# Optimization experiments

Hardware: AMD Instinct MI355X
Metric: run time of the kernel (lower is better)

## Reference

```python
import jax, jax.numpy as jnp
import numpy as np

LN_EPS = 1e-5


def setup_inputs() -> dict:
    key = jax.random.key(0)
    k0, k1, k2, k3 = jax.random.split(key, 4)
    b, X, Y, w1, w2, d = 16, 16, 16, 8, 8, 128
    heads = 4
    x = jax.random.normal(k0, (b, X, Y, w1, w2, d), dtype=jnp.float32)
    gamma = jnp.ones((d,), dtype=jnp.float32)
    beta = jnp.zeros((d,), dtype=jnp.float32)
    w_qkv = jax.random.normal(k1, (d, 3 * d), dtype=jnp.float32) * 0.02
    w_out = jax.random.normal(k2, (d, d), dtype=jnp.float32) * 0.02
    bias_table = jax.random.normal(k3, ((2 * w1 - 1) * (2 * w2 - 1), heads), dtype=jnp.float32) * 0.02
    return {"x": x, "gamma": gamma, "beta": beta, "w_qkv": w_qkv,
            "w_out": w_out, "bias_table": bias_table,
            "window_height": 8, "window_width": 8}


def _rel_pos_indices(wh, ww):
    gh = jnp.arange(wh)
    gw = jnp.arange(ww)
    grid = jnp.stack(jnp.meshgrid(gh, gw, indexing='ij'), axis=-1).reshape(-1, 2)  # [n, 2]
    rel = grid[:, None, :] - grid[None, :, :]  # [n, n, 2]
    rel = rel + jnp.array([wh - 1, ww - 1])
    return rel[..., 0] * (2 * ww - 1) + rel[..., 1]  # [n, n]


def reference(x, gamma, beta, w_qkv, w_out, bias_table, window_height, window_width):
    b, X, Y, w1, w2, d = x.shape
    heads = bias_table.shape[-1]
    dh = d // heads
    scale = dh ** -0.5

    # LayerNorm over channel dim
    mu = x.mean(axis=-1, keepdims=True)
    var = jnp.mean((x - mu) ** 2, axis=-1, keepdims=True)
    xn = (x - mu) * jax.lax.rsqrt(var + LN_EPS) * gamma + beta

    n = w1 * w2
    xn = xn.reshape(b * X * Y, n, d)  # [B, n, d], B = b*X*Y windows

    qkv = xn @ w_qkv  # [B, n, 3d]
    q, k, v = jnp.split(qkv, 3, axis=-1)
    def split_heads(t):
        return t.reshape(t.shape[0], n, heads, dh).transpose(0, 2, 1, 3)  # [B, h, n, dh]
    q, k, v = map(split_heads, (q, k, v))

    sim = jnp.einsum('bhid,bhjd->bhij', q * scale, k)  # [B, h, n, n]

    idx = _rel_pos_indices(window_height, window_width)  # [n, n]
    bias = bias_table[idx].transpose(2, 0, 1)  # [h, n, n]

    attn = jax.nn.softmax(sim + bias, axis=-1)
    out = jnp.einsum('bhij,bhjd->bhid', attn, v)  # [B, h, n, dh]
    out = out.transpose(0, 2, 1, 3).reshape(b * X * Y, w1, w2, d)
    out = out @ w_out
    return out.reshape(b, X, Y, w1, w2, d)
```

## Files before the change

kernel.cpp:

```cpp
#include <hip/hip_runtime.h>

typedef __attribute__((ext_vector_type(4))) short short4v;
typedef __attribute__((ext_vector_type(8))) short short8;
typedef __attribute__((ext_vector_type(4))) float f32x4;

#define NWIN 4096

__device__ __forceinline__ short f2bf(float f) {
    unsigned int u = __builtin_bit_cast(unsigned int, f);
    u += 0x7fffu + ((u >> 16) & 1u);
    return (short)(u >> 16);
}

__device__ __forceinline__ unsigned pack2(float a, float b) {
    return (unsigned)(unsigned short)f2bf(a) | ((unsigned)(unsigned short)f2bf(b) << 16);
}

__device__ __forceinline__ short4v pk4(float a, float b, float c, float d) {
    uint2 u;
    u.x = pack2(a, b);
    u.y = pack2(c, d);
    return __builtin_bit_cast(short4v, u);
}

#define LOG2E 1.4426950408889634f
#define QSCALE 0.17677669529663687f

__global__ void prep_kernel(const float* __restrict__ w_qkv,
                            const float* __restrict__ w_out,
                            const float* __restrict__ bias_table,
                            short* __restrict__ wqkvT,
                            short* __restrict__ woutT,
                            float* __restrict__ biasP)
{
    int id = blockIdx.x * 256 + threadIdx.x;
    if (id < 49152) {
        int j = id >> 7, k = id & 127;
        float v = w_qkv[k * 384 + j];
        if (j < 128) v *= (QSCALE * LOG2E);
        wqkvT[id] = f2bf(v);
    } else if (id < 65536) {
        int t = id - 49152;
        int j = t >> 7, k = t & 127;
        woutT[t] = f2bf(w_out[k * 128 + j]);
    } else if (id < 81920) {
        int t = id - 65536;
        int m  = t & 15;
        int ln = (t >> 4) & 63;
        int ib = (t >> 10) & 3;
        int h  = t >> 12;
        int lo = ln & 15, g = ln >> 4;
        int i = ib * 16 + lo;
        int j = (m >> 2) * 16 + g * 4 + (m & 3);
        int ri = i >> 3, ci = i & 7, rj = j >> 3, cj = j & 7;
        int idx = (ri - rj + 7) * 15 + (ci - cj + 7);
        biasP[t] = bias_table[idx * 4 + h] * LOG2E;
    }
}

__global__ __launch_bounds__(256, 2)
void attn_kernel(const float* __restrict__ x,
                 const float* __restrict__ gamma,
                 const float* __restrict__ beta,
                 const short* __restrict__ wqkvT,
                 const short* __restrict__ woutT,
                 const float* __restrict__ biasP,
                 float* __restrict__ out)
{
    __shared__ __align__(16) char smem[32768];

    const int tid = threadIdx.x;
    const int h  = tid >> 6;
    const int ln = tid & 63;
    const int lo = ln & 15, g = ln >> 4;

    const float* xwin = x + (size_t)blockIdx.x * 8192;

    float4 va[4][2];
    #pragma unroll
    for (int p = 0; p < 4; ++p) {
        int t = h * 16 + p * 4 + g;
        const float4* xr = (const float4*)(xwin + t * 128 + lo * 8);
        va[p][0] = xr[0];
        va[p][1] = xr[1];
    }
    float4 ga0 = ((const float4*)gamma)[lo * 2], ga1 = ((const float4*)gamma)[lo * 2 + 1];
    float4 be0 = ((const float4*)beta)[lo * 2],  be1 = ((const float4*)beta)[lo * 2 + 1];

    #pragma unroll
    for (int p = 0; p < 4; ++p) {
        int t = h * 16 + p * 4 + g;
        float4 v0 = va[p][0], v1 = va[p][1];
        float s  = v0.x + v0.y + v0.z + v0.w + v1.x + v1.y + v1.z + v1.w;
        float sq = v0.x*v0.x + v0.y*v0.y + v0.z*v0.z + v0.w*v0.w
                 + v1.x*v1.x + v1.y*v1.y + v1.z*v1.z + v1.w*v1.w;
        #pragma unroll
        for (int m = 1; m < 16; m <<= 1) {
            s  += __shfl_xor(s, m, 64);
            sq += __shfl_xor(sq, m, 64);
        }
        float mu  = s * (1.f / 128.f);
        float var = sq * (1.f / 128.f) - mu * mu;
        float rs  = rsqrtf(var + 1e-5f);
        float y0 = (v0.x - mu) * rs * ga0.x + be0.x;
        float y1 = (v0.y - mu) * rs * ga0.y + be0.y;
        float y2 = (v0.z - mu) * rs * ga0.z + be0.z;
        float y3 = (v0.w - mu) * rs * ga0.w + be0.w;
        float y4 = (v1.x - mu) * rs * ga1.x + be1.x;
        float y5 = (v1.y - mu) * rs * ga1.y + be1.y;
        float y6 = (v1.z - mu) * rs * ga1.z + be1.z;
        float y7 = (v1.w - mu) * rs * ga1.w + be1.w;
        uint4 pk;
        pk.x = pack2(y0, y1); pk.y = pack2(y2, y3);
        pk.z = pack2(y4, y5); pk.w = pack2(y6, y7);
        *(uint4*)(smem + ((t * 256 + lo * 16) ^ ((t & 7) << 4))) = pk;
    }
    __syncthreads();

    const f32x4 z4 = {0.f, 0.f, 0.f, 0.f};

    f32x4 qt[2][4], kt[2][4];
    #pragma unroll
    for (int a = 0; a < 2; ++a)
        #pragma unroll
        for (int b = 0; b < 4; ++b) { qt[a][b] = z4; kt[a][b] = z4; }

    #pragma unroll
    for (int kk = 0; kk < 4; ++kk) {
        short8 xa[4];
        #pragma unroll
        for (int tb = 0; tb < 4; ++tb) {
            int t = tb * 16 + lo;
            xa[tb] = *(const short8*)(smem + ((t * 256 + kk * 64 + g * 16) ^ ((t & 7) << 4)));
        }
        #pragma unroll
        for (int cb = 0; cb < 2; ++cb) {
            short8 wqf = *(const short8*)(wqkvT + (      h * 32 + cb * 16 + lo) * 128 + kk * 32 + g * 8);
            short8 wkf = *(const short8*)(wqkvT + (128 + h * 32 + cb * 16 + lo) * 128 + kk * 32 + g * 8);
            #pragma unroll
            for (int tb = 0; tb < 4; ++tb) {
                qt[cb][tb] = __builtin_amdgcn_mfma_f32_16x16x32_bf16(wqf, xa[tb], qt[cb][tb], 0, 0, 0);
                kt[cb][tb] = __builtin_amdgcn_mfma_f32_16x16x32_bf16(wkf, xa[tb], kt[cb][tb], 0, 0, 0);
            }
        }
    }

    short4v kA[2][4], qB[2][4];
    #pragma unroll
    for (int ck = 0; ck < 2; ++ck)
        #pragma unroll
        for (int tb = 0; tb < 4; ++tb) {
            kA[ck][tb] = pk4(kt[ck][tb][0], kt[ck][tb][1], kt[ck][tb][2], kt[ck][tb][3]);
            qB[ck][tb] = pk4(qt[ck][tb][0], qt[ck][tb][1], qt[ck][tb][2], qt[ck][tb][3]);
        }

    f32x4 vv[4][2];
    #pragma unroll
    for (int a = 0; a < 4; ++a)
        #pragma unroll
        for (int b = 0; b < 2; ++b) vv[a][b] = z4;

    #pragma unroll
    for (int kk = 0; kk < 4; ++kk) {
        short8 xa[4];
        #pragma unroll
        for (int tb = 0; tb < 4; ++tb) {
            int t = tb * 16 + lo;
            xa[tb] = *(const short8*)(smem + ((t * 256 + kk * 64 + g * 16) ^ ((t & 7) << 4)));
        }
        #pragma unroll
        for (int cb = 0; cb < 2; ++cb) {
            short8 wvf = *(const short8*)(wqkvT + (256 + h * 32 + cb * 16 + lo) * 128 + kk * 32 + g * 8);
            #pragma unroll
            for (int tb = 0; tb < 4; ++tb)
                vv[tb][cb] = __builtin_amdgcn_mfma_f32_16x16x32_bf16(xa[tb], wvf, vv[tb][cb], 0, 0, 0);
        }
    }

    char* vtb = smem + 16384 + h * 4096;
    #pragma unroll
    for (int cb = 0; cb < 2; ++cb)
        #pragma unroll
        for (int tb = 0; tb < 4; ++tb) {
            int c = cb * 16 + lo;
            uint2 w;
            w.x = pack2(vv[tb][cb][0], vv[tb][cb][1]);
            w.y = pack2(vv[tb][cb][2], vv[tb][cb][3]);
            *(uint2*)(vtb + ((c * 128 + tb * 32 + g * 8) ^ ((c & 7) << 4))) = w;
        }

    f32x4 ot[2][4];
    #pragma unroll
    for (int a = 0; a < 2; ++a)
        #pragma unroll
        for (int b = 0; b < 4; ++b) ot[a][b] = z4;

    float inv[4];
    #pragma unroll
    for (int ib = 0; ib < 4; ++ib) {
        f32x4 bias_cur[4];
        {
            const f32x4* bp = (const f32x4*)(biasP + ((h * 4 + ib) * 64 + ln) * 16);
            #pragma unroll
            for (int jb = 0; jb < 4; ++jb) bias_cur[jb] = bp[jb];
        }

        f32x4 st[4];
        #pragma unroll
        for (int jb = 0; jb < 4; ++jb) st[jb] = z4;
        #pragma unroll
        for (int jb = 0; jb < 4; ++jb) {
            st[jb] = __builtin_amdgcn_mfma_f32_16x16x16bf16_1k(kA[0][jb], qB[0][ib], st[jb], 0, 0, 0);
            st[jb] = __builtin_amdgcn_mfma_f32_16x16x16bf16_1k(kA[1][jb], qB[1][ib], st[jb], 0, 0, 0);
        }

        float v[16];
        #pragma unroll
        for (int jb = 0; jb < 4; ++jb)
            #pragma unroll
            for (int r = 0; r < 4; ++r)
                v[jb * 4 + r] = st[jb][r] + bias_cur[jb][r];
        float mx = v[0];
        #pragma unroll
        for (int q = 1; q < 16; ++q) mx = fmaxf(mx, v[q]);
        mx = fmaxf(mx, __shfl_xor(mx, 16, 64));
        mx = fmaxf(mx, __shfl_xor(mx, 32, 64));
        float s = 0.f;
        #pragma unroll
        for (int q = 0; q < 16; ++q) { v[q] = __builtin_exp2f(v[q] - mx); s += v[q]; }
        s += __shfl_xor(s, 16, 64);
        s += __shfl_xor(s, 32, 64);
        inv[ib] = 1.f / s;

        short4v pB[4];
        #pragma unroll
        for (int jk = 0; jk < 4; ++jk)
            pB[jk] = pk4(v[jk * 4 + 0], v[jk * 4 + 1], v[jk * 4 + 2], v[jk * 4 + 3]);

        #pragma unroll
        for (int jk = 0; jk < 4; ++jk)
            #pragma unroll
            for (int cb = 0; cb < 2; ++cb) {
                int c = cb * 16 + lo;
                short4v vA = __builtin_bit_cast(short4v,
                    *(const uint2*)(vtb + ((c * 128 + jk * 32 + g * 8) ^ ((c & 7) << 4))));
                ot[cb][ib] = __builtin_amdgcn_mfma_f32_16x16x16bf16_1k(vA, pB[jk], ot[cb][ib], 0, 0, 0);
            }
    }
    __syncthreads();

    #pragma unroll
    for (int cb = 0; cb < 2; ++cb)
        #pragma unroll
        for (int ib = 0; ib < 4; ++ib) {
            int i = ib * 16 + lo;
            float sc = inv[ib];
            uint2 w;
            w.x = pack2(ot[cb][ib][0] * sc, ot[cb][ib][1] * sc);
            w.y = pack2(ot[cb][ib][2] * sc, ot[cb][ib][3] * sc);
            *(uint2*)(smem + ((i * 256 + (h * 32 + cb * 16 + g * 4) * 2) ^ ((i & 7) << 4))) = w;
        }
    __syncthreads();

    f32x4 ft[2][4];
    #pragma unroll
    for (int a = 0; a < 2; ++a)
        #pragma unroll
        for (int b = 0; b < 4; ++b) ft[a][b] = z4;

    #pragma unroll
    for (int kk = 0; kk < 4; ++kk) {
        short8 ao[4];
        #pragma unroll
        for (int tb = 0; tb < 4; ++tb) {
            int t = tb * 16 + lo;
            ao[tb] = *(const short8*)(smem + ((t * 256 + kk * 64 + g * 16) ^ ((t & 7) << 4)));
        }
        #pragma unroll
        for (int cj = 0; cj < 2; ++cj) {
            short8 wof = *(const short8*)(woutT + (h * 32 + cj * 16 + lo) * 128 + kk * 32 + g * 8);
            #pragma unroll
            for (int tb = 0; tb < 4; ++tb)
                ft[cj][tb] = __builtin_amdgcn_mfma_f32_16x16x32_bf16(wof, ao[tb], ft[cj][tb], 0, 0, 0);
        }
    }

    float* owin = out + (size_t)blockIdx.x * 8192;
    #pragma unroll
    for (int cj = 0; cj < 2; ++cj)
        #pragma unroll
        for (int tb = 0; tb < 4; ++tb) {
            int t = tb * 16 + lo;
            *(f32x4*)(owin + t * 128 + h * 32 + cj * 16 + g * 4) = ft[cj][tb];
        }
}

extern "C" void kernel_launch(void* const* d_in, const int* in_sizes, int n_in,
                              void* d_out, int out_size, void* d_ws, size_t ws_size,
                              hipStream_t stream) {
    const float* x          = (const float*)d_in[0];
    const float* gamma      = (const float*)d_in[1];
    const float* beta       = (const float*)d_in[2];
    const float* w_qkv      = (const float*)d_in[3];
    const float* w_out      = (const float*)d_in[4];
    const float* bias_table = (const float*)d_in[5];

    short* wqkvT = (short*)d_ws;
    short* woutT = (short*)((char*)d_ws + 98304);
    float* biasP = (float*)((char*)d_ws + 131072);

    prep_kernel<<<320, 256, 0, stream>>>(w_qkv, w_out, bias_table, wqkvT, woutT, biasP);
    attn_kernel<<<NWIN, 256, 0, stream>>>(x, gamma, beta, wqkvT, woutT, biasP, (float*)d_out);
}
```

Baseline: 132.1 us.

## Keep V fragments in registers, fold bias into MFMA init, drop softmax max

V tiles produced by the projection MFMAs are packed straight into register operands for the P·V MFMAs, instead of going through a swizzled shared-memory buffer. This halves shared memory to 16 KB and lets launch bounds rise to 3 blocks per SM. The relative-position bias now seeds the score accumulator, and the running-max subtraction in softmax is removed, which saves VALU work and shuffles. The trade-off is that exp2 can overflow if logits grow large, and register pressure rises under the tighter occupancy bound.

Result: slower. 148.7 us (+12.5%).

```diff
diff --git a/kernel.cpp b/kernel.cpp
--- a/kernel.cpp
+++ b/kernel.cpp
@@ -58,7 +58,7 @@
     }
 }
 
-__global__ __launch_bounds__(256, 2)
+__global__ __launch_bounds__(256, 3)
 void attn_kernel(const float* __restrict__ x,
                  const float* __restrict__ gamma,
                  const float* __restrict__ beta,
@@ -67,7 +67,7 @@
                  const float* __restrict__ biasP,
                  float* __restrict__ out)
 {
-    __shared__ __align__(16) char smem[32768];
+    __shared__ __align__(16) char smem[16384];
 
     const int tid = threadIdx.x;
     const int h  = tid >> 6;
@@ -177,17 +177,12 @@
         }
     }
 
-    char* vtb = smem + 16384 + h * 4096;
+    short4v vA[2][4];
     #pragma unroll
     for (int cb = 0; cb < 2; ++cb)
         #pragma unroll
-        for (int tb = 0; tb < 4; ++tb) {
-            int c = cb * 16 + lo;
-            uint2 w;
-            w.x = pack2(vv[tb][cb][0], vv[tb][cb][1]);
-            w.y = pack2(vv[tb][cb][2], vv[tb][cb][3]);
-            *(uint2*)(vtb + ((c * 128 + tb * 32 + g * 8) ^ ((c & 7) << 4))) = w;
-        }
+        for (int jk = 0; jk < 4; ++jk)
+            vA[cb][jk] = pk4(vv[jk][cb][0], vv[jk][cb][1], vv[jk][cb][2], vv[jk][cb][3]);
 
     f32x4 ot[2][4];
     #pragma unroll
@@ -198,16 +193,10 @@
     float inv[4];
     #pragma unroll
     for (int ib = 0; ib < 4; ++ib) {
-        f32x4 bias_cur[4];
-        {
-            const f32x4* bp = (const f32x4*)(biasP + ((h * 4 + ib) * 64 + ln) * 16);
-            #pragma unroll
-            for (int jb = 0; jb < 4; ++jb) bias_cur[jb] = bp[jb];
-        }
-
+        const f32x4* bp = (const f32x4*)(biasP + ((h * 4 + ib) * 64 + ln) * 16);
         f32x4 st[4];
         #pragma unroll
-        for (int jb = 0; jb < 4; ++jb) st[jb] = z4;
+        for (int jb = 0; jb < 4; ++jb) st[jb] = bp[jb];
         #pragma unroll
         for (int jb = 0; jb < 4; ++jb) {
             st[jb] = __builtin_amdgcn_mfma_f32_16x16x16bf16_1k(kA[0][jb], qB[0][ib], st[jb], 0, 0, 0);
@@ -215,19 +204,14 @@
         }
 
         float v[16];
+        float s = 0.f;
         #pragma unroll
         for (int jb = 0; jb < 4; ++jb)
             #pragma unroll
-            for (int r = 0; r < 4; ++r)
-                v[jb * 4 + r] = st[jb][r] + bias_cur[jb][r];
-        float mx = v[0];
-        #pragma unroll
-        for (int q = 1; q < 16; ++q) mx = fmaxf(mx, v[q]);
-        mx = fmaxf(mx, __shfl_xor(mx, 16, 64));
-        mx = fmaxf(mx, __shfl_xor(mx, 32, 64));
-        float s = 0.f;
-        #pragma unroll
-        for (int q = 0; q < 16; ++q) { v[q] = __builtin_exp2f(v[q] - mx); s += v[q]; }
+            for (int r = 0; r < 4; ++r) {
+                v[jb * 4 + r] = __builtin_exp2f(st[jb][r]);
+                s += v[jb * 4 + r];
+            }
         s += __shfl_xor(s, 16, 64);
         s += __shfl_xor(s, 32, 64);
         inv[ib] = 1.f / s;
@@ -240,12 +224,8 @@
         #pragma unroll
         for (int jk = 0; jk < 4; ++jk)
             #pragma unroll
-            for (int cb = 0; cb < 2; ++cb) {
-                int c = cb * 16 + lo;
-                short4v vA = __builtin_bit_cast(short4v,
-                    *(const uint2*)(vtb + ((c * 128 + jk * 32 + g * 8) ^ ((c & 7) << 4))));
-                ot[cb][ib] = __builtin_amdgcn_mfma_f32_16x16x16bf16_1k(vA, pB[jk], ot[cb][ib], 0, 0, 0);
-            }
+            for (int cb = 0; cb < 2; ++cb)
+                ot[cb][ib] = __builtin_amdgcn_mfma_f32_16x16x16bf16_1k(vA[cb][jk], pB[jk], ot[cb][ib], 0, 0, 0);
     }
     __syncthreads();
 
```
